# Performance work log

Measured on AMD Instinct MI355X. Metric: run time of the kernel, lower is better.

Reference implementation:

```python
import jax, jax.numpy as jnp
import numpy as np

EMBED = 512
EXPAND = 1024


def setup_inputs() -> dict:
    key = jax.random.key(0)
    k1, k2, k3, k4, k5 = jax.random.split(key, 5)
    B, C, P, N = 4, EMBED, 16, 1024
    x = jax.random.normal(k1, (B, C, P, N), dtype=jnp.float32)
    # 1x1 conv weights == per-pixel linear maps over the channel dim
    Wqkv = jax.random.normal(k2, (1 + 2 * EXPAND, C), dtype=jnp.float32) * (1.0 / np.sqrt(C))
    bqkv = jax.random.normal(k3, (1 + 2 * EXPAND,), dtype=jnp.float32) * 0.01
    Wout = jax.random.normal(k4, (C, EXPAND), dtype=jnp.float32) * (1.0 / np.sqrt(EXPAND))
    bout = jax.random.normal(k5, (C,), dtype=jnp.float32) * 0.01
    return {"x": x, "Wqkv": Wqkv, "bqkv": bqkv, "Wout": Wout, "bout": bout}


def reference(x, Wqkv, bqkv, Wout, bout):
    # qkv 1x1 conv: (B,C,P,N) -> (B, 1+2E, P, N)
    qkv = jnp.einsum('oc,bcpn->bopn', Wqkv, x) + bqkv[None, :, None, None]
    E = EXPAND
    query = qkv[:, :1]            # (B,1,P,N)
    key_t = qkv[:, 1:1 + E]       # (B,E,P,N)
    value = qkv[:, 1 + E:]        # (B,E,P,N)
    # softmax over patches dim (last axis); attn_dropout p=0.0 -> identity
    context_scores = jax.nn.softmax(query, axis=-1)
    # weighted sum over N, keepdim -> (B,E,P,1)
    context_vector = jnp.sum(key_t * context_scores, axis=-1, keepdims=True)
    # broadcast gate
    out = jax.nn.relu(value) * context_vector  # (B,E,P,N)
    # out 1x1 conv back to embed channels
    out = jnp.einsum('oe,bepn->bopn', Wout, out) + bout[None, :, None, None]
    return out
```

## Files before the change

kernel.cpp:

```cpp
#include <hip/hip_runtime.h>

#define EMBED 512
#define EXPAND 1024
#define PNUM 16
#define NLEN 1024
#define CHW (PNUM * NLEN)
#define SLABS 64

typedef unsigned short u16;
typedef unsigned int u32;
typedef __bf16 bf16x8 __attribute__((ext_vector_type(8)));
typedef u16 u16x8 __attribute__((ext_vector_type(8)));
typedef float f32x4 __attribute__((ext_vector_type(4)));

__device__ __forceinline__ u16 f2bf(float f) {
  u32 u = __builtin_bit_cast(u32, f);
  return (u16)((u + 0x7FFFu + ((u >> 16) & 1u)) >> 16);
}
__device__ __forceinline__ float bf2f(u16 h) {
  return __builtin_bit_cast(float, (u32)h << 16);
}
__device__ __forceinline__ void gld16(const u16* g, u16* l) {
  __builtin_amdgcn_global_load_lds((__attribute__((address_space(1))) void*)g,
                                   (__attribute__((address_space(3))) void*)l,
                                   16, 0, 0);
}
__device__ __forceinline__ f32x4 MFMA(bf16x8 a, bf16x8 b, f32x4 c) {
  return __builtin_amdgcn_mfma_f32_16x16x32_bf16(a, b, c, 0, 0, 0);
}

__global__ __launch_bounds__(256) void k_convert_w(
    const float* __restrict__ Wqkv, const float* __restrict__ Wout,
    u16* __restrict__ WvB, u16* __restrict__ WoutB) {
  const int NV = EXPAND * EMBED;
  int idx = (blockIdx.x * 256 + threadIdx.x) * 4;
  if (idx < NV) {
    float4 v = *(const float4*)(Wqkv + (size_t)(1 + EXPAND) * EMBED + idx);
    uint2 u = make_uint2((u32)f2bf(v.x) | ((u32)f2bf(v.y) << 16),
                         (u32)f2bf(v.z) | ((u32)f2bf(v.w) << 16));
    *(uint2*)(WvB + idx) = u;
  } else {
    int j = idx - NV;
    float4 v = *(const float4*)(Wout + j);
    uint2 u = make_uint2((u32)f2bf(v.x) | ((u32)f2bf(v.y) << 16),
                         (u32)f2bf(v.z) | ((u32)f2bf(v.w) << 16));
    *(uint2*)(WoutB + j) = u;
  }
}

__global__ __launch_bounds__(256) void k_convert_x(
    const float* __restrict__ x, const float* __restrict__ Wqkv,
    float* __restrict__ q, u16* __restrict__ xbT) {
  __shared__ __align__(16) u16 tile[128 * 64];
  __shared__ float qp[256 * 4];
  const int slab = blockIdx.x >> 3, nw = blockIdx.x & 7;
  const int b = slab >> 4, p = slab & 15;
  const int t = threadIdx.x;
  const int c8 = t & 7;
  const int ng = t >> 3;
  const float* xs = x + (size_t)b * (EMBED * CHW) + (size_t)p * NLEN + nw * 128;
  u16* dst = xbT + (size_t)slab * (NLEN * EMBED) + (size_t)(nw * 128) * EMBED;
  float qa[4] = {0.f, 0.f, 0.f, 0.f};

  for (int cc = 0; cc < 8; ++cc) {
    const int cbase = cc * 64;
    float4 v[8];
#pragma unroll
    for (int k = 0; k < 8; ++k)
      v[k] = *(const float4*)(xs + (size_t)(cbase + c8 * 8 + k) * CHW + ng * 4);
    const float* w0 = Wqkv + cbase + c8 * 8;
#pragma unroll
    for (int k = 0; k < 8; ++k) {
      qa[0] += w0[k] * v[k].x;
      qa[1] += w0[k] * v[k].y;
      qa[2] += w0[k] * v[k].z;
      qa[3] += w0[k] * v[k].w;
    }
#pragma unroll
    for (int j = 0; j < 4; ++j) {
      const int nl = ng * 4 + j;
      float e[8];
#pragma unroll
      for (int k = 0; k < 8; ++k)
        e[k] = (j == 0) ? v[k].x : (j == 1) ? v[k].y : (j == 2) ? v[k].z : v[k].w;
      uint4 pk;
      pk.x = (u32)f2bf(e[0]) | ((u32)f2bf(e[1]) << 16);
      pk.y = (u32)f2bf(e[2]) | ((u32)f2bf(e[3]) << 16);
      pk.z = (u32)f2bf(e[4]) | ((u32)f2bf(e[5]) << 16);
      pk.w = (u32)f2bf(e[6]) | ((u32)f2bf(e[7]) << 16);
      *(uint4*)(tile + nl * 64 + ((c8 ^ (nl & 7)) << 3)) = pk;
    }
    __syncthreads();
#pragma unroll
    for (int m = 0; m < 4; ++m) {
      const int s = m * 256 + t;
      const int nl = s >> 3, ch = s & 7;
      uint4 vv = *(const uint4*)(tile + nl * 64 + ((ch ^ (nl & 7)) << 3));
      *(uint4*)(dst + (size_t)nl * EMBED + cbase + ch * 8) = vv;
    }
    __syncthreads();
  }
  qp[t * 4 + 0] = qa[0];
  qp[t * 4 + 1] = qa[1];
  qp[t * 4 + 2] = qa[2];
  qp[t * 4 + 3] = qa[3];
  __syncthreads();
  if (t < 128) {
    float a = 0.f;
#pragma unroll
    for (int o = 0; o < 8; ++o) a += qp[((((t >> 2) << 3) + o) << 2) + (t & 3)];
    q[(size_t)slab * NLEN + nw * 128 + t] = a;
  }
}

__global__ __launch_bounds__(256) void k_attn1(
    const float* __restrict__ q, const u16* __restrict__ xbT,
    float* __restrict__ ypart) {
  __shared__ float red[4];
  __shared__ float sm[256];
  __shared__ float yp[4][512];
  const int slab = blockIdx.x >> 2, qr = blockIdx.x & 3;
  const int t = threadIdx.x, w = t >> 6, l = t & 63;
  const float* qrow = q + (size_t)slab * NLEN;

  float4 q4 = ((const float4*)qrow)[t];
  float m = fmaxf(fmaxf(q4.x, q4.y), fmaxf(q4.z, q4.w));
#pragma unroll
  for (int sh = 32; sh; sh >>= 1) m = fmaxf(m, __shfl_xor(m, sh, 64));
  if (l == 0) red[w] = m;
  __syncthreads();
  float gm = fmaxf(fmaxf(red[0], red[1]), fmaxf(red[2], red[3]));
  float s = __expf(q4.x - gm) + __expf(q4.y - gm) + __expf(q4.z - gm) + __expf(q4.w - gm);
#pragma unroll
  for (int sh = 32; sh; sh >>= 1) s += __shfl_xor(s, sh, 64);
  __syncthreads();
  if (l == 0) red[w] = s;
  __syncthreads();
  float gs = red[0] + red[1] + red[2] + red[3];
  sm[t] = __expf(qrow[qr * 256 + t] - gm) / gs;
  __syncthreads();

  float ya[8] = {0.f, 0.f, 0.f, 0.f, 0.f, 0.f, 0.f, 0.f};
  const u16* xs = xbT + (size_t)slab * (NLEN * EMBED) + (size_t)qr * 256 * EMBED;
  for (int ni = 0; ni < 64; ++ni) {
    const int nloc = ni * 4 + w;
    const float sc = sm[nloc];
    u16x8 v = *(const u16x8*)(xs + (size_t)nloc * EMBED + l * 8);
#pragma unroll
    for (int j = 0; j < 8; ++j) ya[j] += sc * bf2f(v[j]);
  }
#pragma unroll
  for (int j = 0; j < 8; ++j) yp[w][l * 8 + j] = ya[j];
  __syncthreads();
  for (int c = t; c < 512; c += 256)
    ypart[((size_t)slab * 4 + qr) * 512 + c] = yp[0][c] + yp[1][c] + yp[2][c] + yp[3][c];
}

__global__ __launch_bounds__(256) void k_attn2(
    const float* __restrict__ ypart, const float* __restrict__ Wqkv,
    const float* __restrict__ bqkv, float* __restrict__ cv) {
  __shared__ float yl[512];
  const int slab = blockIdx.x >> 2, ec = blockIdx.x & 3;
  const int t = threadIdx.x;
  const int e = ec * 256 + t;
  const float* yb = ypart + (size_t)slab * 4 * 512;
  for (int c = t; c < 512; c += 256)
    yl[c] = yb[c] + yb[512 + c] + yb[1024 + c] + yb[1536 + c];
  __syncthreads();
  const float* wk = Wqkv + (size_t)(1 + e) * EMBED;
  float a = 0.f;
#pragma unroll 4
  for (int c0 = 0; c0 < EMBED; c0 += 4) {
    float4 wv = *(const float4*)(wk + c0);
    a += wv.x * yl[c0] + wv.y * yl[c0 + 1] + wv.z * yl[c0 + 2] + wv.w * yl[c0 + 3];
  }
  cv[(size_t)slab * EXPAND + e] = a + bqkv[1 + e];
}

template <int K, int NT>
__device__ __forceinline__ void gemm256(const u16* __restrict__ Abase,
                                        const u16* __restrict__ Bbase,
                                        u16* lds, f32x4 (&acc)[8][4]) {
  const int t = threadIdx.x;
  const int w = t >> 6, l = t & 63;
  const int wr = w >> 2, wc = w & 3;
  const int lr = l & 15, lj = l >> 4;
  const int rowA0 = wr * 128 + lr;
  const int rowB0 = wc * 64 + lr;

  auto stage = [&](u16* dstBase, const u16* gBase, int kt) {
#pragma unroll
    for (int i = 0; i < 4; ++i) {
      const int s = i * 512 + t;
      const int row = s >> 3;
      const int pch = s & 7;
      gld16(gBase + (size_t)row * K + kt + ((pch ^ (row & 7)) << 3),
            dstBase + s * 8);
    }
  };
  auto rdA = [&](const u16* bufA, int mi, int kc) -> bf16x8 {
    const int row = rowA0 + mi * 16;
    const int ch = kc * 4 + lj;
    return *(const bf16x8*)(bufA + row * 64 + ((ch ^ (row & 7)) << 3));
  };
  auto rdB = [&](const u16* bufB, int ni, int kc) -> bf16x8 {
    const int row = rowB0 + ni * 16;
    const int ch = kc * 4 + lj;
    return *(const bf16x8*)(bufB + row * 64 + ((ch ^ (row & 7)) << 3));
  };

  stage(lds, Abase, 0);
  stage(lds + 16384, Bbase, 0);
  stage(lds + 32768, Abase, 64);
  stage(lds + 49152, Bbase, 64);
  asm volatile("s_waitcnt vmcnt(8)" ::: "memory");
  __builtin_amdgcn_s_barrier();
  __builtin_amdgcn_sched_barrier(0);

#pragma unroll 1
  for (int kt = 0; kt < NT; ++kt) {
    u16* bufA = lds + (kt & 1) * 32768;
    u16* bufB = bufA + 16384;
    const bool st = (kt + 2) < NT;
    const int kt2 = (kt + 2) * 64;
    bf16x8 a0[4][2], a1[4][2], b0[2][2], b1[2][2];

#pragma unroll
    for (int mi = 0; mi < 4; ++mi)
#pragma unroll
      for (int kc = 0; kc < 2; ++kc) a0[mi][kc] = rdA(bufA, mi, kc);
#pragma unroll
    for (int ni = 0; ni < 2; ++ni)
#pragma unroll
      for (int kc = 0; kc < 2; ++kc) b0[ni][kc] = rdB(bufB, ni, kc);
    __builtin_amdgcn_s_barrier();
    __builtin_amdgcn_sched_barrier(0);
    __builtin_amdgcn_s_setprio(1);
#pragma unroll
    for (int mi = 0; mi < 4; ++mi)
#pragma unroll
      for (int ni = 0; ni < 2; ++ni)
#pragma unroll
        for (int kc = 0; kc < 2; ++kc)
          acc[mi][ni] = MFMA(a0[mi][kc], b0[ni][kc], acc[mi][ni]);
    __builtin_amdgcn_s_setprio(0);
    __builtin_amdgcn_sched_barrier(0);
    __builtin_amdgcn_s_barrier();
    __builtin_amdgcn_sched_barrier(0);

#pragma unroll
    for (int ni = 0; ni < 2; ++ni)
#pragma unroll
      for (int kc = 0; kc < 2; ++kc) b1[ni][kc] = rdB(bufB, ni + 2, kc);
    __builtin_amdgcn_s_barrier();
    __builtin_amdgcn_sched_barrier(0);
    __builtin_amdgcn_s_setprio(1);
#pragma unroll
    for (int mi = 0; mi < 4; ++mi)
#pragma unroll
      for (int ni = 0; ni < 2; ++ni)
#pragma unroll
        for (int kc = 0; kc < 2; ++kc)
          acc[mi][ni + 2] = MFMA(a0[mi][kc], b1[ni][kc], acc[mi][ni + 2]);
    __builtin_amdgcn_s_setprio(0);
    __builtin_amdgcn_sched_barrier(0);
    __builtin_amdgcn_s_barrier();
    __builtin_amdgcn_sched_barrier(0);

#pragma unroll
    for (int mi = 0; mi < 4; ++mi)
#pragma unroll
      for (int kc = 0; kc < 2; ++kc) a1[mi][kc] = rdA(bufA, mi + 4, kc);
    if (st) stage(bufB, Bbase, kt2);
    __builtin_amdgcn_s_barrier();
    __builtin_amdgcn_sched_barrier(0);
    __builtin_amdgcn_s_setprio(1);
#pragma unroll
    for (int mi = 0; mi < 4; ++mi)
#pragma unroll
      for (int ni = 0; ni < 2; ++ni)
#pragma unroll
        for (int kc = 0; kc < 2; ++kc)
          acc[mi + 4][ni + 2] = MFMA(a1[mi][kc], b1[ni][kc], acc[mi + 4][ni + 2]);
    __builtin_amdgcn_s_setprio(0);
    __builtin_amdgcn_sched_barrier(0);
    __builtin_amdgcn_s_barrier();
    __builtin_amdgcn_sched_barrier(0);

    if (st) stage(bufA, Abase, kt2);
    __builtin_amdgcn_s_barrier();
    __builtin_amdgcn_sched_barrier(0);
    __builtin_amdgcn_s_setprio(1);
#pragma unroll
    for (int mi = 0; mi < 4; ++mi)
#pragma unroll
      for (int ni = 0; ni < 2; ++ni)
#pragma unroll
        for (int kc = 0; kc < 2; ++kc)
          acc[mi + 4][ni] = MFMA(a1[mi][kc], b0[ni][kc], acc[mi + 4][ni]);
    __builtin_amdgcn_s_setprio(0);
    __builtin_amdgcn_sched_barrier(0);
    if (st)
      asm volatile("s_waitcnt vmcnt(8)" ::: "memory");
    else
      asm volatile("s_waitcnt vmcnt(0)" ::: "memory");
    __builtin_amdgcn_s_barrier();
    __builtin_amdgcn_sched_barrier(0);
  }
}

__global__ __launch_bounds__(512, 2) void k_gemm1(
    const u16* __restrict__ xbT, const u16* __restrict__ WvB,
    const float* __restrict__ bqkv, const float* __restrict__ cv,
    u16* __restrict__ midT) {
  __shared__ __align__(16) u16 lds[65536];
  const int bid = blockIdx.x;
  const int xc = bid & 7, k = bid >> 3;
  const int te = k & 3;
  const int gg = ((k >> 2) << 3) | xc;
  const int slab = gg >> 2, tn = gg & 3;
  const u16* A = xbT + (size_t)slab * (NLEN * EMBED) + (size_t)tn * 256 * EMBED;
  const u16* B = WvB + (size_t)te * 256 * EMBED;
  f32x4 acc[8][4];
  const f32x4 z = {0.f, 0.f, 0.f, 0.f};
#pragma unroll
  for (int i = 0; i < 8; ++i)
#pragma unroll
    for (int j = 0; j < 4; ++j) acc[i][j] = z;
  gemm256<EMBED, 8>(A, B, lds, acc);

  const int t = threadIdx.x, w = t >> 6, l = t & 63;
  const int wr = w >> 2, wc = w & 3;
  const int lr = l & 15, lq4 = (l >> 4) * 4;
#pragma unroll
  for (int ni = 0; ni < 4; ++ni) {
    const int col = wc * 64 + ni * 16 + lr;
    const int e = te * 256 + col;
    const float bv = bqkv[1 + EXPAND + e];
    const float cve = cv[(size_t)slab * EXPAND + e];
#pragma unroll
    for (int mi = 0; mi < 8; ++mi) {
      const int nr = wr * 128 + mi * 16 + lq4;
#pragma unroll
      for (int r = 0; r < 4; ++r) {
        float v = acc[mi][ni][r] + bv;
        v = v > 0.f ? v * cve : 0.f;
        const int row = nr + r;
        lds[row * 256 + ((((col >> 3) ^ (row & 7)) << 3) | (col & 7))] = f2bf(v);
      }
    }
  }
  __syncthreads();
  u16* mt = midT + (size_t)slab * (NLEN * EXPAND) + (size_t)te * 256;
#pragma unroll
  for (int it = 0; it < 16; ++it) {
    const int row = w * 32 + it * 2 + (l >> 5);
    const int ch = (l & 31) ^ (row & 7);
    uint4 v = *(const uint4*)(lds + row * 256 + ch * 8);
    *(uint4*)(mt + (size_t)(tn * 256 + row) * EXPAND + (l & 31) * 8) = v;
  }
}

__global__ __launch_bounds__(512, 2) void k_gemm2(
    const u16* __restrict__ midT, const u16* __restrict__ WoutB,
    const float* __restrict__ bout, float* __restrict__ out) {
  __shared__ __align__(16) u16 lds[65536];
  const int bid = blockIdx.x;
  const int xc = bid & 7, k = bid >> 3;
  const int to = k & 1;
  const int gg = ((k >> 1) << 3) | xc;
  const int slab = gg >> 2, tn = gg & 3;
  const int b = slab >> 4, p = slab & 15;
  const u16* A = midT + (size_t)slab * (NLEN * EXPAND) + (size_t)tn * 256 * EXPAND;
  const u16* B = WoutB + (size_t)to * 256 * EXPAND;
  f32x4 acc[8][4];
  const f32x4 z = {0.f, 0.f, 0.f, 0.f};
#pragma unroll
  for (int i = 0; i < 8; ++i)
#pragma unroll
    for (int j = 0; j < 4; ++j) acc[i][j] = z;
  gemm256<EXPAND, 16>(A, B, lds, acc);

  const int t = threadIdx.x, w = t >> 6, l = t & 63;
  const int wr = w >> 2, wc = w & 3;
  const int lr = l & 15, lq4 = (l >> 4) * 4;
  float* ob = out + (size_t)b * (EMBED * CHW) + (size_t)p * NLEN;
#pragma unroll
  for (int ni = 0; ni < 4; ++ni) {
    const int o = to * 256 + wc * 64 + ni * 16 + lr;
    const float bo = bout[o];
#pragma unroll
    for (int mi = 0; mi < 8; ++mi) {
      const int nr = tn * 256 + wr * 128 + mi * 16 + lq4;
      float4 v;
      v.x = acc[mi][ni][0] + bo;
      v.y = acc[mi][ni][1] + bo;
      v.z = acc[mi][ni][2] + bo;
      v.w = acc[mi][ni][3] + bo;
      *(float4*)(ob + (size_t)o * CHW + nr) = v;
    }
  }
}

extern "C" void kernel_launch(void* const* d_in, const int* in_sizes, int n_in,
                              void* d_out, int out_size, void* d_ws, size_t ws_size,
                              hipStream_t stream) {
  const float* x = (const float*)d_in[0];
  const float* Wqkv = (const float*)d_in[1];
  const float* bqkv = (const float*)d_in[2];
  const float* Wout = (const float*)d_in[3];
  const float* bout = (const float*)d_in[4];
  float* out = (float*)d_out;

  char* ws = (char*)d_ws;
  u16* xbT = (u16*)ws;
  u16* WvB = (u16*)(ws + 67108864);
  u16* WoutB = (u16*)(ws + 68157440);
  float* q = (float*)(ws + 69206016);
  float* cv = (float*)(ws + 69468160);
  u16* midT = (u16*)(ws + 69730304);
  float* ypart = (float*)(ws + 69730304);

  k_convert_w<<<1024, 256, 0, stream>>>(Wqkv, Wout, WvB, WoutB);
  k_convert_x<<<512, 256, 0, stream>>>(x, Wqkv, q, xbT);
  k_attn1<<<256, 256, 0, stream>>>(q, xbT, ypart);
  k_attn2<<<256, 256, 0, stream>>>(ypart, Wqkv, bqkv, cv);
  k_gemm1<<<1024, 512, 0, stream>>>(xbT, WvB, bqkv, cv, midT);
  k_gemm2<<<512, 512, 0, stream>>>(midT, WoutB, bout, out);
}
```

Baseline: 267.7 us.

## Prefetch next k-tile LDS fragments during current MFMA phases in GEMM mainloop

Restructures the double-buffered GEMM main loop so the first A and B register fragments for the next k-tile are read from LDS during the current tile's later MFMA phases, rather than at the start of each iteration. The loop is unrolled by two with swapped register sets for B0, and the vmcnt wait is tightened and moved earlier. This is meant to hide LDS read latency behind MFMA work and remove one barrier-bound read phase per tile. In exchange it raises register pressure and assumes NT is even.

```diff
diff --git a/kernel.cpp b/kernel.cpp
--- a/kernel.cpp
+++ b/kernel.cpp
@@ -209,59 +209,49 @@
     return *(const bf16x8*)(bufB + row * 64 + ((ch ^ (row & 7)) << 3));
   };
 
-  stage(lds, Abase, 0);
-  stage(lds + 16384, Bbase, 0);
-  stage(lds + 32768, Abase, 64);
-  stage(lds + 49152, Bbase, 64);
+  u16* bA0 = lds;
+  u16* bB0 = lds + 16384;
+  u16* bA1 = lds + 32768;
+  u16* bB1 = lds + 49152;
+
+  stage(bA0, Abase, 0);
+  stage(bB0, Bbase, 0);
+  stage(bA1, Abase, 64);
+  stage(bB1, Bbase, 64);
   asm volatile("s_waitcnt vmcnt(8)" ::: "memory");
   __builtin_amdgcn_s_barrier();
   __builtin_amdgcn_sched_barrier(0);
 
-#pragma unroll 1
-  for (int kt = 0; kt < NT; ++kt) {
-    u16* bufA = lds + (kt & 1) * 32768;
-    u16* bufB = bufA + 16384;
+  bf16x8 a0[4][2], a1[4][2], b1f[2][2], b0X[2][2], b0Y[2][2];
+#pragma unroll
+  for (int mi = 0; mi < 4; ++mi)
+#pragma unroll
+    for (int kc = 0; kc < 2; ++kc) a0[mi][kc] = rdA(bA0, mi, kc);
+#pragma unroll
+  for (int ni = 0; ni < 2; ++ni)
+#pragma unroll
+    for (int kc = 0; kc < 2; ++kc) b0X[ni][kc] = rdB(bB0, ni, kc);
+
+  auto group = [&](int kt, u16* bufA, u16* bufB, u16* nbufA, u16* nbufB,
+                   bf16x8 (&b0c)[2][2], bf16x8 (&b0n)[2][2]) {
     const bool st = (kt + 2) < NT;
+    const bool rd = (kt + 1) < NT;
     const int kt2 = (kt + 2) * 64;
-    bf16x8 a0[4][2], a1[4][2], b0[2][2], b1[2][2];
-
+
+#pragma unroll
+    for (int ni = 0; ni < 2; ++ni)
+#pragma unroll
+      for (int kc = 0; kc < 2; ++kc) b1f[ni][kc] = rdB(bufB, ni + 2, kc);
+    __builtin_amdgcn_s_barrier();
+    __builtin_amdgcn_sched_barrier(0);
+    __builtin_amdgcn_s_setprio(1);
 #pragma unroll
     for (int mi = 0; mi < 4; ++mi)
 #pragma unroll
-      for (int kc = 0; kc < 2; ++kc) a0[mi][kc] = rdA(bufA, mi, kc);
-#pragma unroll
-    for (int ni = 0; ni < 2; ++ni)
-#pragma unroll
-      for (int kc = 0; kc < 2; ++kc) b0[ni][kc] = rdB(bufB, ni, kc);
-    __builtin_amdgcn_s_barrier();
-    __builtin_amdgcn_sched_barrier(0);
-    __builtin_amdgcn_s_setprio(1);
-#pragma unroll
-    for (int mi = 0; mi < 4; ++mi)
-#pragma unroll
       for (int ni = 0; ni < 2; ++ni)
 #pragma unroll
         for (int kc = 0; kc < 2; ++kc)
-          acc[mi][ni] = MFMA(a0[mi][kc], b0[ni][kc], acc[mi][ni]);
-    __builtin_amdgcn_s_setprio(0);
-    __builtin_amdgcn_sched_barrier(0);
-    __builtin_amdgcn_s_barrier();
-    __builtin_amdgcn_sched_barrier(0);
-
-#pragma unroll
-    for (int ni = 0; ni < 2; ++ni)
-#pragma unroll
-      for (int kc = 0; kc < 2; ++kc) b1[ni][kc] = rdB(bufB, ni + 2, kc);
-    __builtin_amdgcn_s_barrier();
-    __builtin_amdgcn_sched_barrier(0);
-    __builtin_amdgcn_s_setprio(1);
-#pragma unroll
-    for (int mi = 0; mi < 4; ++mi)
-#pragma unroll
-      for (int ni = 0; ni < 2; ++ni)
-#pragma unroll
-        for (int kc = 0; kc < 2; ++kc)
-          acc[mi][ni + 2] = MFMA(a0[mi][kc], b1[ni][kc], acc[mi][ni + 2]);
+          acc[mi][ni] = MFMA(a0[mi][kc], b0c[ni][kc], acc[mi][ni]);
     __builtin_amdgcn_s_setprio(0);
     __builtin_amdgcn_sched_barrier(0);
     __builtin_amdgcn_s_barrier();
@@ -281,31 +271,64 @@
       for (int ni = 0; ni < 2; ++ni)
 #pragma unroll
         for (int kc = 0; kc < 2; ++kc)
-          acc[mi + 4][ni + 2] = MFMA(a1[mi][kc], b1[ni][kc], acc[mi + 4][ni + 2]);
+          acc[mi][ni + 2] = MFMA(a0[mi][kc], b1f[ni][kc], acc[mi][ni + 2]);
     __builtin_amdgcn_s_setprio(0);
     __builtin_amdgcn_sched_barrier(0);
     __builtin_amdgcn_s_barrier();
     __builtin_amdgcn_sched_barrier(0);
 
-    if (st) stage(bufA, Abase, kt2);
-    __builtin_amdgcn_s_barrier();
-    __builtin_amdgcn_sched_barrier(0);
-    __builtin_amdgcn_s_setprio(1);
-#pragma unroll
-    for (int mi = 0; mi < 4; ++mi)
-#pragma unroll
-      for (int ni = 0; ni < 2; ++ni)
-#pragma unroll
-        for (int kc = 0; kc < 2; ++kc)
-          acc[mi + 4][ni] = MFMA(a1[mi][kc], b0[ni][kc], acc[mi + 4][ni]);
-    __builtin_amdgcn_s_setprio(0);
-    __builtin_amdgcn_sched_barrier(0);
     if (st)
-      asm volatile("s_waitcnt vmcnt(8)" ::: "memory");
+      asm volatile("s_waitcnt vmcnt(4)" ::: "memory");
     else
       asm volatile("s_waitcnt vmcnt(0)" ::: "memory");
-    __builtin_amdgcn_s_barrier();
-    __builtin_amdgcn_sched_barrier(0);
+    if (rd) {
+#pragma unroll
+      for (int ni = 0; ni < 2; ++ni)
+#pragma unroll
+        for (int kc = 0; kc < 2; ++kc) b0n[ni][kc] = rdB(nbufB, ni, kc);
+    }
+    __builtin_amdgcn_s_barrier();
+    __builtin_amdgcn_sched_barrier(0);
+    __builtin_amdgcn_s_setprio(1);
+#pragma unroll
+    for (int mi = 0; mi < 4; ++mi)
+#pragma unroll
+      for (int ni = 0; ni < 2; ++ni)
+#pragma unroll
+        for (int kc = 0; kc < 2; ++kc)
+          acc[mi + 4][ni + 2] = MFMA(a1[mi][kc], b1f[ni][kc], acc[mi + 4][ni + 2]);
+    __builtin_amdgcn_s_setprio(0);
+    __builtin_amdgcn_sched_barrier(0);
+    __builtin_amdgcn_s_barrier();
+    __builtin_amdgcn_sched_barrier(0);
+
+    if (rd) {
+#pragma unroll
+      for (int mi = 0; mi < 4; ++mi)
+#pragma unroll
+        for (int kc = 0; kc < 2; ++kc) a0[mi][kc] = rdA(nbufA, mi, kc);
+    }
+    if (st) stage(bufA, Abase, kt2);
+    __builtin_amdgcn_s_barrier();
+    __builtin_amdgcn_sched_barrier(0);
+    __builtin_amdgcn_s_setprio(1);
+#pragma unroll
+    for (int mi = 0; mi < 4; ++mi)
+#pragma unroll
+      for (int ni = 0; ni < 2; ++ni)
+#pragma unroll
+        for (int kc = 0; kc < 2; ++kc)
+          acc[mi + 4][ni] = MFMA(a1[mi][kc], b0c[ni][kc], acc[mi + 4][ni]);
+    __builtin_amdgcn_s_setprio(0);
+    __builtin_amdgcn_sched_barrier(0);
+    __builtin_amdgcn_s_barrier();
+    __builtin_amdgcn_sched_barrier(0);
+  };
+
+#pragma unroll 1
+  for (int kt = 0; kt < NT; kt += 2) {
+    group(kt, bA0, bB0, bA1, bB1, b0X, b0Y);
+    group(kt + 1, bA1, bB1, bA0, bB0, b0Y, b0X);
   }
 }
 
```

Result: slower. 646.7 us (+141.6%).

## Split GEMM tile staging into half-chunks spread across MFMA phases

Applied to the files above, without the earlier changes.

The global-to-LDS staging of each A and B k-tile is broken into two-load chunks issued at four points in the main loop instead of two large bursts. Part of the next A tile (rows 64-127 and 192-255) is loaded one iteration later, into the other buffer, just after it stops being read. The wait threshold drops from 8 to 6 outstanding loads. The aim is to spread memory traffic more evenly over the MFMA phases and overlap it better, at the cost of more complex buffer-hazard reasoning.

```diff
diff --git a/kernel.cpp b/kernel.cpp
--- a/kernel.cpp
+++ b/kernel.cpp
@@ -188,12 +188,16 @@
   const int rowA0 = wr * 128 + lr;
   const int rowB0 = wc * 64 + lr;
 
-  auto stage = [&](u16* dstBase, const u16* gBase, int kt) {
-#pragma unroll
-    for (int i = 0; i < 4; ++i) {
-      const int s = i * 512 + t;
-      const int row = s >> 3;
-      const int pch = s & 7;
+  auto stage2 = [&](u16* dstBase, const u16* gBase, int kt, int s0, int s1) {
+    {
+      const int s = s0 + t;
+      const int row = s >> 3, pch = s & 7;
+      gld16(gBase + (size_t)row * K + kt + ((pch ^ (row & 7)) << 3),
+            dstBase + s * 8);
+    }
+    {
+      const int s = s1 + t;
+      const int row = s >> 3, pch = s & 7;
       gld16(gBase + (size_t)row * K + kt + ((pch ^ (row & 7)) << 3),
             dstBase + s * 8);
     }
@@ -209,11 +213,19 @@
     return *(const bf16x8*)(bufB + row * 64 + ((ch ^ (row & 7)) << 3));
   };
 
-  stage(lds, Abase, 0);
-  stage(lds + 16384, Bbase, 0);
-  stage(lds + 32768, Abase, 64);
-  stage(lds + 49152, Bbase, 64);
-  asm volatile("s_waitcnt vmcnt(8)" ::: "memory");
+  u16* bA0 = lds;
+  u16* bB0 = lds + 16384;
+  u16* bA1 = lds + 32768;
+  u16* bB1 = lds + 49152;
+
+  stage2(bA0, Abase, 0, 0, 1024);
+  stage2(bB0, Bbase, 0, 0, 512);
+  stage2(bB0, Bbase, 0, 1024, 1536);
+  stage2(bA0, Abase, 0, 512, 1536);
+  stage2(bA1, Abase, 64, 0, 1024);
+  stage2(bB1, Bbase, 64, 0, 512);
+  stage2(bB1, Bbase, 64, 1024, 1536);
+  asm volatile("s_waitcnt vmcnt(6)" ::: "memory");
   __builtin_amdgcn_s_barrier();
   __builtin_amdgcn_sched_barrier(0);
 
@@ -221,8 +233,10 @@
   for (int kt = 0; kt < NT; ++kt) {
     u16* bufA = lds + (kt & 1) * 32768;
     u16* bufB = bufA + 16384;
-    const bool st = (kt + 2) < NT;
-    const int kt2 = (kt + 2) * 64;
+    u16* nbufA = lds + (((kt + 1) & 1)) * 32768;
+    const bool st1 = (kt + 1) < NT;
+    const bool st2 = (kt + 2) < NT;
+    const int k1 = (kt + 1) * 64, k2 = (kt + 2) * 64;
     bf16x8 a0[4][2], a1[4][2], b0[2][2], b1[2][2];
 
 #pragma unroll
@@ -233,6 +247,7 @@
     for (int ni = 0; ni < 2; ++ni)
 #pragma unroll
       for (int kc = 0; kc < 2; ++kc) b0[ni][kc] = rdB(bufB, ni, kc);
+    if (st1) stage2(nbufA, Abase, k1, 512, 1536);
     __builtin_amdgcn_s_barrier();
     __builtin_amdgcn_sched_barrier(0);
     __builtin_amdgcn_s_setprio(1);
@@ -252,6 +267,7 @@
     for (int ni = 0; ni < 2; ++ni)
 #pragma unroll
       for (int kc = 0; kc < 2; ++kc) b1[ni][kc] = rdB(bufB, ni + 2, kc);
+    if (st2) stage2(bufA, Abase, k2, 0, 1024);
     __builtin_amdgcn_s_barrier();
     __builtin_amdgcn_sched_barrier(0);
     __builtin_amdgcn_s_setprio(1);
@@ -271,7 +287,7 @@
     for (int mi = 0; mi < 4; ++mi)
 #pragma unroll
       for (int kc = 0; kc < 2; ++kc) a1[mi][kc] = rdA(bufA, mi + 4, kc);
-    if (st) stage(bufB, Bbase, kt2);
+    if (st2) stage2(bufB, Bbase, k2, 0, 512);
     __builtin_amdgcn_s_barrier();
     __builtin_amdgcn_sched_barrier(0);
     __builtin_amdgcn_s_setprio(1);
@@ -287,7 +303,7 @@
     __builtin_amdgcn_s_barrier();
     __builtin_amdgcn_sched_barrier(0);
 
-    if (st) stage(bufA, Abase, kt2);
+    if (st2) stage2(bufB, Bbase, k2, 1024, 1536);
     __builtin_amdgcn_s_barrier();
     __builtin_amdgcn_sched_barrier(0);
     __builtin_amdgcn_s_setprio(1);
@@ -300,8 +316,8 @@
           acc[mi + 4][ni] = MFMA(a1[mi][kc], b0[ni][kc], acc[mi + 4][ni]);
     __builtin_amdgcn_s_setprio(0);
     __builtin_amdgcn_sched_barrier(0);
-    if (st)
-      asm volatile("s_waitcnt vmcnt(8)" ::: "memory");
+    if (st2)
+      asm volatile("s_waitcnt vmcnt(6)" ::: "memory");
     else
       asm volatile("s_waitcnt vmcnt(0)" ::: "memory");
     __builtin_amdgcn_s_barrier();
```

After: 267.2 us. About the same (-0.2%).

## Make both GEMMs persistent with continuous cross-tile prefetch pipelines

Applied to the files above, without the earlier changes.

k_gemm1 and k_gemm2 become persistent kernels launched with 256 blocks, each looping over several output tiles. The double-buffered LDS prefetch continues across tile boundaries, so the next tile's loads overlap the current tile's tail, and each tile is written out by an in-loop epilogue. In gemm1 the operand roles are swapped so the weight slice stays fixed per block. Its epilogue now writes packed bf16 straight to global instead of transposing through LDS, with a precomputed bias vector stored in the reused q workspace. The changes also drop the sched_barrier hints and move the weight conversion later in the launch order. The trade-offs are less coalesced epilogue stores, possible scheduler reordering, and fewer blocks to balance the work.

```diff
diff --git a/kernel.cpp b/kernel.cpp
--- a/kernel.cpp
+++ b/kernel.cpp
@@ -31,7 +31,8 @@
 
 __global__ __launch_bounds__(256) void k_convert_w(
     const float* __restrict__ Wqkv, const float* __restrict__ Wout,
-    u16* __restrict__ WvB, u16* __restrict__ WoutB) {
+    const float* __restrict__ bqkv, u16* __restrict__ WvB,
+    u16* __restrict__ WoutB, float* __restrict__ bvv) {
   const int NV = EXPAND * EMBED;
   int idx = (blockIdx.x * 256 + threadIdx.x) * 4;
   if (idx < NV) {
@@ -46,6 +47,10 @@
                          (u32)f2bf(v.z) | ((u32)f2bf(v.w) << 16));
     *(uint2*)(WoutB + j) = u;
   }
+  if (blockIdx.x == 0) {
+    for (int i = threadIdx.x; i < EXPAND; i += 256)
+      bvv[i] = bqkv[1 + EXPAND + i];
+  }
 }
 
 __global__ __launch_bounds__(256) void k_convert_x(
@@ -177,52 +182,71 @@
   cv[(size_t)slab * EXPAND + e] = a + bqkv[1 + e];
 }
 
-template <int K, int NT>
-__device__ __forceinline__ void gemm256(const u16* __restrict__ Abase,
-                                        const u16* __restrict__ Bbase,
-                                        u16* lds, f32x4 (&acc)[8][4]) {
+__global__ __launch_bounds__(512, 2) void k_gemm1(
+    const u16* __restrict__ xbT, const u16* __restrict__ WvB,
+    const float* __restrict__ bvv, const float* __restrict__ cv,
+    u16* __restrict__ midT) {
+  __shared__ __align__(16) u16 lds[65536];
+  const int bid = blockIdx.x;
   const int t = threadIdx.x;
   const int w = t >> 6, l = t & 63;
   const int wr = w >> 2, wc = w & 3;
-  const int lr = l & 15, lj = l >> 4;
-  const int rowA0 = wr * 128 + lr;
-  const int rowB0 = wc * 64 + lr;
-
-  auto stage = [&](u16* dstBase, const u16* gBase, int kt) {
+  const int lr = l & 15, lj = l >> 4, lq4 = (l >> 4) * 4;
+  const int te = (bid >> 3) & 3;
+  const u16* Ab = WvB + (size_t)te * (256 * EMBED);
+
+  auto ggOf = [&](int f) -> int {
+    const int tid = ((f >> 3) << 8) + bid;
+    return (((tid >> 3) >> 2) << 3) | (tid & 7);
+  };
+  auto stageA = [&](int fs) {
+    u16* dst = lds + (fs & 1) * 32768;
+    const int kc = (fs & 7) * 64;
 #pragma unroll
     for (int i = 0; i < 4; ++i) {
       const int s = i * 512 + t;
-      const int row = s >> 3;
-      const int pch = s & 7;
-      gld16(gBase + (size_t)row * K + kt + ((pch ^ (row & 7)) << 3),
-            dstBase + s * 8);
+      const int row = s >> 3, pch = s & 7;
+      gld16(Ab + (size_t)row * EMBED + kc + ((pch ^ (row & 7)) << 3), dst + s * 8);
+    }
+  };
+  auto stageB = [&](int fs) {
+    const u16* gB = xbT + (size_t)ggOf(fs) * (256 * EMBED);
+    u16* dst = lds + (fs & 1) * 32768 + 16384;
+    const int kc = (fs & 7) * 64;
+#pragma unroll
+    for (int i = 0; i < 4; ++i) {
+      const int s = i * 512 + t;
+      const int row = s >> 3, pch = s & 7;
+      gld16(gB + (size_t)row * EMBED + kc + ((pch ^ (row & 7)) << 3), dst + s * 8);
     }
   };
   auto rdA = [&](const u16* bufA, int mi, int kc) -> bf16x8 {
-    const int row = rowA0 + mi * 16;
+    const int row = wr * 128 + mi * 16 + lr;
     const int ch = kc * 4 + lj;
     return *(const bf16x8*)(bufA + row * 64 + ((ch ^ (row & 7)) << 3));
   };
   auto rdB = [&](const u16* bufB, int ni, int kc) -> bf16x8 {
-    const int row = rowB0 + ni * 16;
+    const int row = wc * 64 + ni * 16 + lr;
     const int ch = kc * 4 + lj;
     return *(const bf16x8*)(bufB + row * 64 + ((ch ^ (row & 7)) << 3));
   };
 
-  stage(lds, Abase, 0);
-  stage(lds + 16384, Bbase, 0);
-  stage(lds + 32768, Abase, 64);
-  stage(lds + 49152, Bbase, 64);
+  stageA(0); stageB(0); stageA(1); stageB(1);
   asm volatile("s_waitcnt vmcnt(8)" ::: "memory");
   __builtin_amdgcn_s_barrier();
-  __builtin_amdgcn_sched_barrier(0);
+
+  f32x4 acc[8][4];
+  const f32x4 z = {0.f, 0.f, 0.f, 0.f};
+#pragma unroll
+  for (int i = 0; i < 8; ++i)
+#pragma unroll
+    for (int j = 0; j < 4; ++j) acc[i][j] = z;
 
 #pragma unroll 1
-  for (int kt = 0; kt < NT; ++kt) {
-    u16* bufA = lds + (kt & 1) * 32768;
+  for (int f = 0; f < 32; ++f) {
+    u16* bufA = lds + (f & 1) * 32768;
     u16* bufB = bufA + 16384;
-    const bool st = (kt + 2) < NT;
-    const int kt2 = (kt + 2) * 64;
+    const bool st = (f + 2) < 32;
     bf16x8 a0[4][2], a1[4][2], b0[2][2], b1[2][2];
 
 #pragma unroll
@@ -234,7 +258,6 @@
 #pragma unroll
       for (int kc = 0; kc < 2; ++kc) b0[ni][kc] = rdB(bufB, ni, kc);
     __builtin_amdgcn_s_barrier();
-    __builtin_amdgcn_sched_barrier(0);
     __builtin_amdgcn_s_setprio(1);
 #pragma unroll
     for (int mi = 0; mi < 4; ++mi)
@@ -244,16 +267,13 @@
         for (int kc = 0; kc < 2; ++kc)
           acc[mi][ni] = MFMA(a0[mi][kc], b0[ni][kc], acc[mi][ni]);
     __builtin_amdgcn_s_setprio(0);
-    __builtin_amdgcn_sched_barrier(0);
-    __builtin_amdgcn_s_barrier();
-    __builtin_amdgcn_sched_barrier(0);
+    __builtin_amdgcn_s_barrier();
 
 #pragma unroll
     for (int ni = 0; ni < 2; ++ni)
 #pragma unroll
       for (int kc = 0; kc < 2; ++kc) b1[ni][kc] = rdB(bufB, ni + 2, kc);
     __builtin_amdgcn_s_barrier();
-    __builtin_amdgcn_sched_barrier(0);
     __builtin_amdgcn_s_setprio(1);
 #pragma unroll
     for (int mi = 0; mi < 4; ++mi)
@@ -263,17 +283,14 @@
         for (int kc = 0; kc < 2; ++kc)
           acc[mi][ni + 2] = MFMA(a0[mi][kc], b1[ni][kc], acc[mi][ni + 2]);
     __builtin_amdgcn_s_setprio(0);
-    __builtin_amdgcn_sched_barrier(0);
-    __builtin_amdgcn_s_barrier();
-    __builtin_amdgcn_sched_barrier(0);
+    __builtin_amdgcn_s_barrier();
 
 #pragma unroll
     for (int mi = 0; mi < 4; ++mi)
 #pragma unroll
       for (int kc = 0; kc < 2; ++kc) a1[mi][kc] = rdA(bufA, mi + 4, kc);
-    if (st) stage(bufB, Bbase, kt2);
-    __builtin_amdgcn_s_barrier();
-    __builtin_amdgcn_sched_barrier(0);
+    if (st) stageB(f + 2);
+    __builtin_amdgcn_s_barrier();
     __builtin_amdgcn_s_setprio(1);
 #pragma unroll
     for (int mi = 0; mi < 4; ++mi)
@@ -283,13 +300,10 @@
         for (int kc = 0; kc < 2; ++kc)
           acc[mi + 4][ni + 2] = MFMA(a1[mi][kc], b1[ni][kc], acc[mi + 4][ni + 2]);
     __builtin_amdgcn_s_setprio(0);
-    __builtin_amdgcn_sched_barrier(0);
-    __builtin_amdgcn_s_barrier();
-    __builtin_amdgcn_sched_barrier(0);
-
-    if (st) stage(bufA, Abase, kt2);
-    __builtin_amdgcn_s_barrier();
-    __builtin_amdgcn_sched_barrier(0);
+    __builtin_amdgcn_s_barrier();
+
+    if (st) stageA(f + 2);
+    __builtin_amdgcn_s_barrier();
     __builtin_amdgcn_s_setprio(1);
 #pragma unroll
     for (int mi = 0; mi < 4; ++mi)
@@ -299,65 +313,39 @@
         for (int kc = 0; kc < 2; ++kc)
           acc[mi + 4][ni] = MFMA(a1[mi][kc], b0[ni][kc], acc[mi + 4][ni]);
     __builtin_amdgcn_s_setprio(0);
-    __builtin_amdgcn_sched_barrier(0);
     if (st)
       asm volatile("s_waitcnt vmcnt(8)" ::: "memory");
     else
       asm volatile("s_waitcnt vmcnt(0)" ::: "memory");
     __builtin_amdgcn_s_barrier();
-    __builtin_amdgcn_sched_barrier(0);
-  }
-}
-
-__global__ __launch_bounds__(512, 2) void k_gemm1(
-    const u16* __restrict__ xbT, const u16* __restrict__ WvB,
-    const float* __restrict__ bqkv, const float* __restrict__ cv,
-    u16* __restrict__ midT) {
-  __shared__ __align__(16) u16 lds[65536];
-  const int bid = blockIdx.x;
-  const int xc = bid & 7, k = bid >> 3;
-  const int te = k & 3;
-  const int gg = ((k >> 2) << 3) | xc;
-  const int slab = gg >> 2, tn = gg & 3;
-  const u16* A = xbT + (size_t)slab * (NLEN * EMBED) + (size_t)tn * 256 * EMBED;
-  const u16* B = WvB + (size_t)te * 256 * EMBED;
-  f32x4 acc[8][4];
-  const f32x4 z = {0.f, 0.f, 0.f, 0.f};
-#pragma unroll
-  for (int i = 0; i < 8; ++i)
-#pragma unroll
-    for (int j = 0; j < 4; ++j) acc[i][j] = z;
-  gemm256<EMBED, 8>(A, B, lds, acc);
-
-  const int t = threadIdx.x, w = t >> 6, l = t & 63;
-  const int wr = w >> 2, wc = w & 3;
-  const int lr = l & 15, lq4 = (l >> 4) * 4;
-#pragma unroll
-  for (int ni = 0; ni < 4; ++ni) {
-    const int col = wc * 64 + ni * 16 + lr;
-    const int e = te * 256 + col;
-    const float bv = bqkv[1 + EXPAND + e];
-    const float cve = cv[(size_t)slab * EXPAND + e];
-#pragma unroll
-    for (int mi = 0; mi < 8; ++mi) {
-      const int nr = wr * 128 + mi * 16 + lq4;
-#pragma unroll
-      for (int r = 0; r < 4; ++r) {
-        float v = acc[mi][ni][r] + bv;
-        v = v > 0.f ? v * cve : 0.f;
-        const int row = nr + r;
-        lds[row * 256 + ((((col >> 3) ^ (row & 7)) << 3) | (col & 7))] = f2bf(v);
+
+    if ((f & 7) == 7) {
+      const int gg = ggOf(f);
+      const int slab = gg >> 2;
+      u16* mt = midT + (size_t)gg * (256 * EXPAND);
+#pragma unroll
+      for (int mi = 0; mi < 8; ++mi) {
+        const int e0 = te * 256 + wr * 128 + mi * 16 + lq4;
+        const float4 cv4 = *(const float4*)(cv + (size_t)slab * EXPAND + e0);
+        const float4 bv4 = *(const float4*)(bvv + e0);
+#pragma unroll
+        for (int ni = 0; ni < 4; ++ni) {
+          const int nl = wc * 64 + ni * 16 + lr;
+          float v0 = acc[mi][ni][0] + bv4.x; v0 = v0 > 0.f ? v0 * cv4.x : 0.f;
+          float v1 = acc[mi][ni][1] + bv4.y; v1 = v1 > 0.f ? v1 * cv4.y : 0.f;
+          float v2 = acc[mi][ni][2] + bv4.z; v2 = v2 > 0.f ? v2 * cv4.z : 0.f;
+          float v3 = acc[mi][ni][3] + bv4.w; v3 = v3 > 0.f ? v3 * cv4.w : 0.f;
+          uint2 pk;
+          pk.x = (u32)f2bf(v0) | ((u32)f2bf(v1) << 16);
+          pk.y = (u32)f2bf(v2) | ((u32)f2bf(v3) << 16);
+          *(uint2*)(mt + (size_t)nl * EXPAND + e0) = pk;
+        }
       }
-    }
-  }
-  __syncthreads();
-  u16* mt = midT + (size_t)slab * (NLEN * EXPAND) + (size_t)te * 256;
-#pragma unroll
-  for (int it = 0; it < 16; ++it) {
-    const int row = w * 32 + it * 2 + (l >> 5);
-    const int ch = (l & 31) ^ (row & 7);
-    uint4 v = *(const uint4*)(lds + row * 256 + ch * 8);
-    *(uint4*)(mt + (size_t)(tn * 256 + row) * EXPAND + (l & 31) * 8) = v;
+#pragma unroll
+      for (int i = 0; i < 8; ++i)
+#pragma unroll
+        for (int j = 0; j < 4; ++j) acc[i][j] = z;
+    }
   }
 }
 
@@ -366,38 +354,161 @@
     const float* __restrict__ bout, float* __restrict__ out) {
   __shared__ __align__(16) u16 lds[65536];
   const int bid = blockIdx.x;
-  const int xc = bid & 7, k = bid >> 3;
-  const int to = k & 1;
-  const int gg = ((k >> 1) << 3) | xc;
-  const int slab = gg >> 2, tn = gg & 3;
-  const int b = slab >> 4, p = slab & 15;
-  const u16* A = midT + (size_t)slab * (NLEN * EXPAND) + (size_t)tn * 256 * EXPAND;
-  const u16* B = WoutB + (size_t)to * 256 * EXPAND;
+  const int t = threadIdx.x;
+  const int w = t >> 6, l = t & 63;
+  const int wr = w >> 2, wc = w & 3;
+  const int lr = l & 15, lj = l >> 4, lq4 = (l >> 4) * 4;
+  const int to = (bid >> 3) & 1;
+  const u16* Bb = WoutB + (size_t)to * (256 * EXPAND);
+
+  auto ggOf = [&](int f) -> int {
+    const int tid = ((f >> 4) << 8) + bid;
+    return (((tid >> 3) >> 1) << 3) | (tid & 7);
+  };
+  auto stageA = [&](int fs) {
+    const u16* gA = midT + (size_t)ggOf(fs) * (256 * EXPAND);
+    u16* dst = lds + (fs & 1) * 32768;
+    const int kc = (fs & 15) * 64;
+#pragma unroll
+    for (int i = 0; i < 4; ++i) {
+      const int s = i * 512 + t;
+      const int row = s >> 3, pch = s & 7;
+      gld16(gA + (size_t)row * EXPAND + kc + ((pch ^ (row & 7)) << 3), dst + s * 8);
+    }
+  };
+  auto stageB = [&](int fs) {
+    u16* dst = lds + (fs & 1) * 32768 + 16384;
+    const int kc = (fs & 15) * 64;
+#pragma unroll
+    for (int i = 0; i < 4; ++i) {
+      const int s = i * 512 + t;
+      const int row = s >> 3, pch = s & 7;
+      gld16(Bb + (size_t)row * EXPAND + kc + ((pch ^ (row & 7)) << 3), dst + s * 8);
+    }
+  };
+  auto rdA = [&](const u16* bufA, int mi, int kc) -> bf16x8 {
+    const int row = wr * 128 + mi * 16 + lr;
+    const int ch = kc * 4 + lj;
+    return *(const bf16x8*)(bufA + row * 64 + ((ch ^ (row & 7)) << 3));
+  };
+  auto rdB = [&](const u16* bufB, int ni, int kc) -> bf16x8 {
+    const int row = wc * 64 + ni * 16 + lr;
+    const int ch = kc * 4 + lj;
+    return *(const bf16x8*)(bufB + row * 64 + ((ch ^ (row & 7)) << 3));
+  };
+
+  stageA(0); stageB(0); stageA(1); stageB(1);
+  asm volatile("s_waitcnt vmcnt(8)" ::: "memory");
+  __builtin_amdgcn_s_barrier();
+
   f32x4 acc[8][4];
   const f32x4 z = {0.f, 0.f, 0.f, 0.f};
 #pragma unroll
   for (int i = 0; i < 8; ++i)
 #pragma unroll
     for (int j = 0; j < 4; ++j) acc[i][j] = z;
-  gemm256<EXPAND, 16>(A, B, lds, acc);
-
-  const int t = threadIdx.x, w = t >> 6, l = t & 63;
-  const int wr = w >> 2, wc = w & 3;
-  const int lr = l & 15, lq4 = (l >> 4) * 4;
-  float* ob = out + (size_t)b * (EMBED * CHW) + (size_t)p * NLEN;
-#pragma unroll
-  for (int ni = 0; ni < 4; ++ni) {
-    const int o = to * 256 + wc * 64 + ni * 16 + lr;
-    const float bo = bout[o];
-#pragma unroll
-    for (int mi = 0; mi < 8; ++mi) {
-      const int nr = tn * 256 + wr * 128 + mi * 16 + lq4;
-      float4 v;
-      v.x = acc[mi][ni][0] + bo;
-      v.y = acc[mi][ni][1] + bo;
-      v.z = acc[mi][ni][2] + bo;
-      v.w = acc[mi][ni][3] + bo;
-      *(float4*)(ob + (size_t)o * CHW + nr) = v;
+
+#pragma unroll 1
+  for (int f = 0; f < 32; ++f) {
+    u16* bufA = lds + (f & 1) * 32768;
+    u16* bufB = bufA + 16384;
+    const bool st = (f + 2) < 32;
+    bf16x8 a0[4][2], a1[4][2], b0[2][2], b1[2][2];
+
+#pragma unroll
+    for (int mi = 0; mi < 4; ++mi)
+#pragma unroll
+      for (int kc = 0; kc < 2; ++kc) a0[mi][kc] = rdA(bufA, mi, kc);
+#pragma unroll
+    for (int ni = 0; ni < 2; ++ni)
+#pragma unroll
+      for (int kc = 0; kc < 2; ++kc) b0[ni][kc] = rdB(bufB, ni, kc);
+    __builtin_amdgcn_s_barrier();
+    __builtin_amdgcn_s_setprio(1);
+#pragma unroll
+    for (int mi = 0; mi < 4; ++mi)
+#pragma unroll
+      for (int ni = 0; ni < 2; ++ni)
+#pragma unroll
+        for (int kc = 0; kc < 2; ++kc)
+          acc[mi][ni] = MFMA(a0[mi][kc], b0[ni][kc], acc[mi][ni]);
+    __builtin_amdgcn_s_setprio(0);
+    __builtin_amdgcn_s_barrier();
+
+#pragma unroll
+    for (int ni = 0; ni < 2; ++ni)
+#pragma unroll
+      for (int kc = 0; kc < 2; ++kc) b1[ni][kc] = rdB(bufB, ni + 2, kc);
+    __builtin_amdgcn_s_barrier();
+    __builtin_amdgcn_s_setprio(1);
+#pragma unroll
+    for (int mi = 0; mi < 4; ++mi)
+#pragma unroll
+      for (int ni = 0; ni < 2; ++ni)
+#pragma unroll
+        for (int kc = 0; kc < 2; ++kc)
+          acc[mi][ni + 2] = MFMA(a0[mi][kc], b1[ni][kc], acc[mi][ni + 2]);
+    __builtin_amdgcn_s_setprio(0);
+    __builtin_amdgcn_s_barrier();
+
+#pragma unroll
+    for (int mi = 0; mi < 4; ++mi)
+#pragma unroll
+      for (int kc = 0; kc < 2; ++kc) a1[mi][kc] = rdA(bufA, mi + 4, kc);
+    if (st) stageB(f + 2);
+    __builtin_amdgcn_s_barrier();
+    __builtin_amdgcn_s_setprio(1);
+#pragma unroll
+    for (int mi = 0; mi < 4; ++mi)
+#pragma unroll
+      for (int ni = 0; ni < 2; ++ni)
+#pragma unroll
+        for (int kc = 0; kc < 2; ++kc)
+          acc[mi + 4][ni + 2] = MFMA(a1[mi][kc], b1[ni][kc], acc[mi + 4][ni + 2]);
+    __builtin_amdgcn_s_setprio(0);
+    __builtin_amdgcn_s_barrier();
+
+    if (st) stageA(f + 2);
+    __builtin_amdgcn_s_barrier();
+    __builtin_amdgcn_s_setprio(1);
+#pragma unroll
+    for (int mi = 0; mi < 4; ++mi)
+#pragma unroll
+      for (int ni = 0; ni < 2; ++ni)
+#pragma unroll
+        for (int kc = 0; kc < 2; ++kc)
+          acc[mi + 4][ni] = MFMA(a1[mi][kc], b0[ni][kc], acc[mi + 4][ni]);
+    __builtin_amdgcn_s_setprio(0);
+    if (st)
+      asm volatile("s_waitcnt vmcnt(8)" ::: "memory");
+    else
+      asm volatile("s_waitcnt vmcnt(0)" ::: "memory");
+    __builtin_amdgcn_s_barrier();
+
+    if ((f & 15) == 15) {
+      const int gg = ggOf(f);
+      const int slab = gg >> 2, tn = gg & 3;
+      const int b = slab >> 4, p = slab & 15;
+      float* ob = out + (size_t)b * (EMBED * CHW) + (size_t)p * NLEN;
+#pragma unroll
+      for (int ni = 0; ni < 4; ++ni) {
+        const int o = to * 256 + wc * 64 + ni * 16 + lr;
+        const float bo = bout[o];
+#pragma unroll
+        for (int mi = 0; mi < 8; ++mi) {
+          const int nr = tn * 256 + wr * 128 + mi * 16 + lq4;
+          float4 v;
+          v.x = acc[mi][ni][0] + bo;
+          v.y = acc[mi][ni][1] + bo;
+          v.z = acc[mi][ni][2] + bo;
+          v.w = acc[mi][ni][3] + bo;
+          *(float4*)(ob + (size_t)o * CHW + nr) = v;
+        }
+      }
+#pragma unroll
+      for (int i = 0; i < 8; ++i)
+#pragma unroll
+        for (int j = 0; j < 4; ++j) acc[i][j] = z;
     }
   }
 }
@@ -420,11 +531,12 @@
   float* cv = (float*)(ws + 69468160);
   u16* midT = (u16*)(ws + 69730304);
   float* ypart = (float*)(ws + 69730304);
-
-  k_convert_w<<<1024, 256, 0, stream>>>(Wqkv, Wout, WvB, WoutB);
+  float* bvv = (float*)(ws + 69206016);
+
   k_convert_x<<<512, 256, 0, stream>>>(x, Wqkv, q, xbT);
   k_attn1<<<256, 256, 0, stream>>>(q, xbT, ypart);
+  k_convert_w<<<1024, 256, 0, stream>>>(Wqkv, Wout, bqkv, WvB, WoutB, bvv);
   k_attn2<<<256, 256, 0, stream>>>(ypart, Wqkv, bqkv, cv);
-  k_gemm1<<<1024, 512, 0, stream>>>(xbT, WvB, bqkv, cv, midT);
-  k_gemm2<<<512, 512, 0, stream>>>(midT, WoutB, bout, out);
-}
+  k_gemm1<<<256, 512, 0, stream>>>(xbT, WvB, bvv, cv, midT);
+  k_gemm2<<<256, 512, 0, stream>>>(midT, WoutB, bout, out);
+}
```

New measurement: 267.8 us. No clear change (+0.0%).
